# Kernel tuning notes

Measured on AMD Instinct MI355X. Metric: run time of the kernel, lower is better.

The kernel has to match this reference:

```python
import jax, jax.numpy as jnp
import numpy as np

EMBED_DIM = 1024
NUM_HEADS = 16
HEAD_DIM = EMBED_DIM // NUM_HEADS


def setup_inputs() -> dict:
    key = jax.random.key(0)
    ks = jax.random.split(key, 5)
    B, S, D = 2, 2048, EMBED_DIM
    scale_w = 1.0 / np.sqrt(D)
    x = jax.random.normal(ks[0], (B, S, D), dtype=jnp.float32)
    Wq = jax.random.normal(ks[1], (D, D), dtype=jnp.float32) * scale_w
    Wk = jax.random.normal(ks[2], (D, D), dtype=jnp.float32) * scale_w
    Wv = jax.random.normal(ks[3], (D, D), dtype=jnp.float32) * scale_w
    Wo = jax.random.normal(ks[4], (D, D), dtype=jnp.float32) * scale_w
    return {"x": x, "Wq": Wq, "Wk": Wk, "Wv": Wv, "Wo": Wo}


def reference(x, Wq, Wk, Wv, Wo):
    B, S, D = x.shape
    H, Dh = NUM_HEADS, HEAD_DIM
    scale = 1.0 / jnp.sqrt(jnp.asarray(Dh, dtype=x.dtype))

    def split_heads(t):
        return t.reshape(B, S, H, Dh).transpose(0, 2, 1, 3)  # [B,H,S,Dh]

    q = split_heads(x @ Wq)
    k = split_heads(x @ Wk)
    v = split_heads(x @ Wv)

    scores = jnp.einsum("bhqd,bhkd->bhqk", q, k) * scale
    causal = jnp.tril(jnp.ones((S, S), dtype=bool))[None, None]
    scores = jnp.where(causal, scores, jnp.asarray(-1e9, dtype=scores.dtype))
    weights = jax.nn.softmax(scores, axis=-1)
    attn = jnp.einsum("bhqk,bhkd->bhqd", weights, v)
    attn = attn.transpose(0, 2, 1, 3).reshape(B, S, D)
    return attn @ Wo
```

## Files before the change

kernel.cpp:

```cpp
#include <hip/hip_runtime.h>
#include <cstdint>

typedef __bf16 bf16;
typedef __bf16 bf16x2 __attribute__((ext_vector_type(2)));
typedef __bf16 bf16x4 __attribute__((ext_vector_type(4)));
typedef __bf16 bf16x8 __attribute__((ext_vector_type(8)));
typedef float f32x4 __attribute__((ext_vector_type(4)));

constexpr int S = 2048, D = 1024, H = 16, HD = 64, B = 2;
constexpr size_t TSZ = (size_t)B * H * S * HD;

__device__ __forceinline__ f32x4 mfma16(bf16x8 a, bf16x8 b, f32x4 c) {
  return __builtin_amdgcn_mfma_f32_16x16x32_bf16(a, b, c, 0, 0, 0);
}

__device__ __forceinline__ void gl_lds16(const bf16* g, bf16* s) {
  __builtin_amdgcn_global_load_lds((__attribute__((address_space(1))) void*)g,
                                   (__attribute__((address_space(3))) void*)s,
                                   16, 0, 0);
}

__global__ __launch_bounds__(256) void prep_all(const float* __restrict__ x,
                                                const float* __restrict__ W0,
                                                const float* __restrict__ W1,
                                                const float* __restrict__ W2,
                                                const float* __restrict__ W3,
                                                bf16* __restrict__ xb,
                                                bf16* __restrict__ Wt) {
  __shared__ __align__(16) bf16 Lt[64][68];
  const int bid = blockIdx.x, t = threadIdx.x;
  if (bid < 2048) {
    const size_t i = (size_t)bid * 256 + t;
    const float4 a = ((const float4*)x)[2 * i];
    const float4 b = ((const float4*)x)[2 * i + 1];
    bf16x8 o = {(bf16)a.x, (bf16)a.y, (bf16)a.z, (bf16)a.w,
                (bf16)b.x, (bf16)b.y, (bf16)b.z, (bf16)b.w};
    *(bf16x8*)&xb[i * 8] = o;
    return;
  }
  const int r = bid - 2048;
  const int z = r >> 8, rest = r & 255;
  const float* W = z == 0 ? W0 : z == 1 ? W1 : z == 2 ? W2 : W3;
  const int k0 = (rest & 15) * 64, n0 = (rest >> 4) * 64;
  const int tr = t >> 4, tc = (t & 15) * 4;
#pragma unroll
  for (int p = 0; p < 4; ++p) {
    const int rr = 16 * p + tr;
    const float4 v = *(const float4*)&W[(size_t)(k0 + rr) * D + n0 + tc];
    Lt[tc + 0][rr] = (bf16)v.x;
    Lt[tc + 1][rr] = (bf16)v.y;
    Lt[tc + 2][rr] = (bf16)v.z;
    Lt[tc + 3][rr] = (bf16)v.w;
  }
  __syncthreads();
#pragma unroll
  for (int p = 0; p < 4; ++p) {
    const int n = 16 * p + tr;
    const bf16x4 o = *(const bf16x4*)&Lt[n][tc];
    *(bf16x4*)&Wt[((size_t)z * D + n0 + n) * D + k0 + tc] = o;
  }
}

template <int MODE, int BNT>
__global__ __launch_bounds__(256) void gemm_bt(const bf16* __restrict__ A,
                                               const bf16* __restrict__ Bt,
                                               void* __restrict__ Cp) {
  constexpr int K = 1024;
  constexpr int NI = BNT / 32;
  __shared__ __align__(16) bf16 As[128 * 64];
  __shared__ __align__(16) bf16 Bs[BNT * 64];

  const int bid = blockIdx.x, nwg = gridDim.x;
  const int lg = (bid & 7) * (nwg >> 3) + (bid >> 3);
  const int bm = (lg & 31) * 128;
  const int bn = (lg >> 5) * BNT;

  const int t = threadIdx.x, l = t & 63, w = t >> 6;
  const int c = l & 15, g = l >> 4, cx = c & 7;
  const int lrow = l >> 3;
  const int srcc = ((l & 7) ^ lrow) << 3;
  const int wm = (w >> 1) * 64, wn = (w & 1) * (BNT / 2);

  f32x4 acc[4][NI] = {};

  for (int kt = 0; kt < K / 64; ++kt) {
    const int k0 = kt * 64;
    __syncthreads();
#pragma unroll
    for (int i = 0; i < 4; ++i) {
      const int ci = i * 4 + w;
      const int row = ci * 8 + lrow;
      gl_lds16(A + (size_t)(bm + row) * K + k0 + srcc, As + ci * 512 + l * 8);
    }
#pragma unroll
    for (int i = 0; i < BNT / 32; ++i) {
      const int ci = i * 4 + w;
      const int row = ci * 8 + lrow;
      gl_lds16(Bt + (size_t)(bn + row) * K + k0 + srcc, Bs + ci * 512 + l * 8);
    }
    __syncthreads();

    bf16x8 af[4][2], bfv[NI][2];
#pragma unroll
    for (int mi = 0; mi < 4; ++mi) {
      const int row = wm + mi * 16 + c;
#pragma unroll
      for (int kh = 0; kh < 2; ++kh)
        af[mi][kh] = *(const bf16x8*)&As[row * 64 + (((kh * 4 + g) ^ cx) << 3)];
    }
#pragma unroll
    for (int ni = 0; ni < NI; ++ni) {
      const int row = wn + ni * 16 + c;
#pragma unroll
      for (int kh = 0; kh < 2; ++kh)
        bfv[ni][kh] = *(const bf16x8*)&Bs[row * 64 + (((kh * 4 + g) ^ cx) << 3)];
    }
#pragma unroll
    for (int mi = 0; mi < 4; ++mi)
#pragma unroll
      for (int ni = 0; ni < NI; ++ni) {
        acc[mi][ni] = mfma16(af[mi][0], bfv[ni][0], acc[mi][ni]);
        acc[mi][ni] = mfma16(af[mi][1], bfv[ni][1], acc[mi][ni]);
      }
  }

#pragma unroll
  for (int mi = 0; mi < 4; ++mi)
#pragma unroll
    for (int ni = 0; ni < NI; ++ni)
#pragma unroll
      for (int r = 0; r < 4; ++r) {
        const int m = bm + wm + mi * 16 + 4 * g + r;
        const int n = bn + wn + ni * 16 + c;
        const float v = acc[mi][ni][r];
        if constexpr (MODE == 0) {
          const int which = n >> 10, nn = n & 1023;
          const int h = nn >> 6, d = nn & 63;
          const int bb = m >> 11, s = m & 2047;
          ((bf16*)Cp)[which * TSZ + ((((size_t)bb * H + h) * S + s) << 6) + d] =
              (bf16)v;
        } else {
          ((float*)Cp)[(size_t)m * D + n] = v;
        }
      }
}

__global__ __launch_bounds__(256, 4) void attn9(const bf16* __restrict__ Q,
                                                const bf16* __restrict__ Kg,
                                                const bf16* __restrict__ Vg,
                                                bf16* __restrict__ O) {
  __shared__ __align__(16) bf16 Ks[64 * 64];
  __shared__ __align__(16) bf16 Vt[64 * 64];
  __shared__ __align__(16) bf16 Pb[4][16 * 64];

  const int bid = blockIdx.x;
  const int qt = 31 - (bid >> 5);
  const int bh = bid & 31;
  const int t = threadIdx.x, l = t & 63, w = t >> 6;
  const int c = l & 15, g = l >> 4, cx = c & 7;
  const int bb = bh >> 4, h = bh & 15;
  const float SC = 0.18033688011112042f;
  const float THRS = 44.3614195558365f;

  const bf16* Kbase = Kg + (size_t)bh * S * HD;
  const bf16* Vbase = Vg + (size_t)bh * S * HD;

  const int q0 = qt * 64;
  const int qglob = q0 + 16 * w + c;
  const bf16* Qrow = Q + ((size_t)bh * S + qglob) * HD;
  const bf16x8 qf0 = *(const bf16x8*)&Qrow[g * 8];
  const bf16x8 qf1 = *(const bf16x8*)&Qrow[32 + g * 8];

  const int kv0 = t >> 3, dg0 = t & 7;
  const int kv1 = kv0 + 32;
  const int p2 = t & 31, dgv = t >> 5;

  bf16x8 ka0 = *(const bf16x8*)&Kbase[kv0 * 64 + dg0 * 8];
  bf16x8 ka1 = *(const bf16x8*)&Kbase[kv1 * 64 + dg0 * 8];
  bf16x8 va0 = *(const bf16x8*)&Vbase[(2 * p2) * 64 + dgv * 8];
  bf16x8 va1 = *(const bf16x8*)&Vbase[(2 * p2 + 1) * 64 + dgv * 8];

  f32x4 oacc[4] = {};
  float mrun = -1e30f, lrun = 0.f;

  for (int kt = 0; kt <= qt; ++kt) {
    __builtin_amdgcn_s_barrier();
    __builtin_amdgcn_sched_barrier(0);

    *(bf16x8*)&Ks[kv0 * 64 + ((dg0 ^ (kv0 & 7)) << 3)] = ka0;
    *(bf16x8*)&Ks[kv1 * 64 + ((dg0 ^ (kv1 & 7)) << 3)] = ka1;
#pragma unroll
    for (int i = 0; i < 8; ++i) {
      const int vd = 8 * dgv + i;
      bf16x2 pr2 = {va0[i], va1[i]};
      *(bf16x2*)&Vt[vd * 64 + (((p2 >> 2) ^ i) << 3) + ((p2 & 3) << 1)] = pr2;
    }
    bf16x8 kn0 = ka0, kn1 = ka1, vn0 = va0, vn1 = va1;
    if (kt < qt) {
      const bf16* Kt = Kbase + (size_t)(kt + 1) * 64 * HD;
      const bf16* Vs = Vbase + (size_t)(kt + 1) * 64 * HD;
      kn0 = *(const bf16x8*)&Kt[kv0 * 64 + dg0 * 8];
      kn1 = *(const bf16x8*)&Kt[kv1 * 64 + dg0 * 8];
      vn0 = *(const bf16x8*)&Vs[(2 * p2) * 64 + dgv * 8];
      vn1 = *(const bf16x8*)&Vs[(2 * p2 + 1) * 64 + dgv * 8];
    }
    asm volatile("s_waitcnt lgkmcnt(0)" ::: "memory");
    __builtin_amdgcn_s_barrier();
    __builtin_amdgcn_sched_barrier(0);

    f32x4 st[4];
    __builtin_amdgcn_s_setprio(1);
#pragma unroll
    for (int ct = 0; ct < 4; ++ct) {
      const int krow = ct * 16 + c;
      const bf16x8 kf0 = *(const bf16x8*)&Ks[krow * 64 + ((g ^ cx) << 3)];
      const bf16x8 kf1 = *(const bf16x8*)&Ks[krow * 64 + (((4 + g) ^ cx) << 3)];
      f32x4 z = {};
      z = mfma16(kf0, qf0, z);
      st[ct] = mfma16(kf1, qf1, z);
    }
    __builtin_amdgcn_s_setprio(0);

    if (kt == qt) {
#pragma unroll
      for (int ct = 0; ct < 4; ++ct)
#pragma unroll
        for (int r = 0; r < 4; ++r)
          if (kt * 64 + ct * 16 + 4 * g + r > qglob) st[ct][r] = -1e30f;
    }

    float tm[4];
#pragma unroll
    for (int ct = 0; ct < 4; ++ct)
      tm[ct] = fmaxf(fmaxf(st[ct][0], st[ct][1]), fmaxf(st[ct][2], st[ct][3]));
    float mt = fmaxf(fmaxf(tm[0], tm[1]), fmaxf(tm[2], tm[3]));
    mt = fmaxf(mt, __shfl_xor(mt, 16));
    mt = fmaxf(mt, __shfl_xor(mt, 32));
    if (!__all(mt <= mrun + THRS)) {
      const float mnew = fmaxf(mrun, mt);
      const float fac = __builtin_amdgcn_exp2f((mrun - mnew) * SC);
      lrun *= fac;
#pragma unroll
      for (int ct = 0; ct < 4; ++ct)
#pragma unroll
        for (int r = 0; r < 4; ++r) oacc[ct][r] *= fac;
      mrun = mnew;
    }
    float p[4][4];
    float sq[4];
#pragma unroll
    for (int ct = 0; ct < 4; ++ct) {
#pragma unroll
      for (int r = 0; r < 4; ++r)
        p[ct][r] = __builtin_amdgcn_exp2f((st[ct][r] - mrun) * SC);
      sq[ct] = (p[ct][0] + p[ct][1]) + (p[ct][2] + p[ct][3]);
    }
    lrun += (sq[0] + sq[1]) + (sq[2] + sq[3]);

    bf16* Pw = &Pb[w][0];
#pragma unroll
    for (int ct = 0; ct < 4; ++ct)
#pragma unroll
      for (int pr = 0; pr < 2; ++pr) {
        const int ch = (2 * ct + (g >> 1)) ^ cx;
        bf16x2 pk = {(bf16)p[ct][2 * pr], (bf16)p[ct][2 * pr + 1]};
        *(bf16x2*)&Pw[c * 64 + ch * 8 + (g & 1) * 4 + pr * 2] = pk;
      }
    const bf16x8 pa0 = *(const bf16x8*)&Pw[c * 64 + ((g ^ cx) << 3)];
    const bf16x8 pa1 = *(const bf16x8*)&Pw[c * 64 + (((4 + g) ^ cx) << 3)];

    __builtin_amdgcn_s_setprio(1);
#pragma unroll
    for (int ct = 0; ct < 4; ++ct) {
      const int vrow = ct * 16 + c;
      const bf16x8 vt0 = *(const bf16x8*)&Vt[vrow * 64 + ((g ^ cx) << 3)];
      const bf16x8 vt1 = *(const bf16x8*)&Vt[vrow * 64 + (((4 + g) ^ cx) << 3)];
      oacc[ct] = mfma16(vt0, pa0, oacc[ct]);
      oacc[ct] = mfma16(vt1, pa1, oacc[ct]);
    }
    __builtin_amdgcn_s_setprio(0);

    ka0 = kn0; ka1 = kn1; va0 = vn0; va1 = vn1;
  }

  float lt = lrun;
  lt += __shfl_xor(lt, 16);
  lt += __shfl_xor(lt, 32);
  const float inv = 1.f / lt;
  bf16* Orow = O + ((size_t)bb * S + qglob) * D + h * 64;
#pragma unroll
  for (int ct = 0; ct < 4; ++ct)
#pragma unroll
    for (int pr = 0; pr < 2; ++pr) {
      bf16x2 pk = {(bf16)(oacc[ct][2 * pr] * inv),
                   (bf16)(oacc[ct][2 * pr + 1] * inv)};
      *(bf16x2*)&Orow[ct * 16 + 4 * g + 2 * pr] = pk;
    }
}

extern "C" void kernel_launch(void* const* d_in, const int* in_sizes, int n_in,
                              void* d_out, int out_size, void* d_ws, size_t ws_size,
                              hipStream_t stream) {
  const float* x  = (const float*)d_in[0];
  const float* Wq = (const float*)d_in[1];
  const float* Wk = (const float*)d_in[2];
  const float* Wv = (const float*)d_in[3];
  const float* Wo = (const float*)d_in[4];
  float* out = (float*)d_out;

  bf16* xb  = (bf16*)d_ws;
  bf16* Wt  = xb + (size_t)B * S * D;
  bf16* QKV = Wt + (size_t)4 * D * D;
  bf16* Ab  = QKV + 3 * TSZ;

  prep_all<<<3072, 256, 0, stream>>>(x, Wq, Wk, Wv, Wo, xb, Wt);
  gemm_bt<0, 128><<<768, 256, 0, stream>>>(xb, Wt, QKV);
  attn9<<<1024, 256, 0, stream>>>(QKV, QKV + TSZ, QKV + 2 * TSZ, Ab);
  gemm_bt<1, 64><<<512, 256, 0, stream>>>(Ab, Wt + (size_t)3 * D * D, out);
}
```

Before: 100.5 us.

## Split long causal attention rows across two KV halves with a merge kernel

```diff
diff --git a/kernel.cpp b/kernel.cpp
--- a/kernel.cpp
+++ b/kernel.cpp
@@ -145,20 +145,22 @@
       }
 }
 
-__global__ __launch_bounds__(256, 4) void attn9(const bf16* __restrict__ Q,
-                                                const bf16* __restrict__ Kg,
-                                                const bf16* __restrict__ Vg,
-                                                bf16* __restrict__ O) {
+__global__ __launch_bounds__(256, 4) void attn10(const bf16* __restrict__ Q,
+                                                 const bf16* __restrict__ Kg,
+                                                 const bf16* __restrict__ Vg,
+                                                 float* __restrict__ Pp) {
   __shared__ __align__(16) bf16 Ks[64 * 64];
   __shared__ __align__(16) bf16 Vt[64 * 64];
-  __shared__ __align__(16) bf16 Pb[4][16 * 64];
 
   const int bid = blockIdx.x;
-  const int qt = 31 - (bid >> 5);
-  const int bh = bid & 31;
+  const int bh = bid & 31, e = bid >> 5;
+  int qt, kvA, kvB, half;
+  if (e < 16)      { qt = 31 - e; half = 0; kvA = 0;             kvB = (qt + 2) >> 1; }
+  else if (e < 32) { qt = 47 - e; half = 1; kvA = (qt + 2) >> 1; kvB = qt + 1; }
+  else             { qt = 47 - e; half = 0; kvA = 0;             kvB = qt + 1; }
+
   const int t = threadIdx.x, l = t & 63, w = t >> 6;
   const int c = l & 15, g = l >> 4, cx = c & 7;
-  const int bb = bh >> 4, h = bh & 15;
   const float SC = 0.18033688011112042f;
   const float THRS = 44.3614195558365f;
 
@@ -174,16 +176,22 @@
   const int kv0 = t >> 3, dg0 = t & 7;
   const int kv1 = kv0 + 32;
   const int p2 = t & 31, dgv = t >> 5;
-
-  bf16x8 ka0 = *(const bf16x8*)&Kbase[kv0 * 64 + dg0 * 8];
-  bf16x8 ka1 = *(const bf16x8*)&Kbase[kv1 * 64 + dg0 * 8];
-  bf16x8 va0 = *(const bf16x8*)&Vbase[(2 * p2) * 64 + dgv * 8];
-  bf16x8 va1 = *(const bf16x8*)&Vbase[(2 * p2 + 1) * 64 + dgv * 8];
+  const int hv = p2 >> 4;
+  const int gv = (p2 >> 1) & 3;
+  const int jv = ((p2 >> 3) & 1) * 4 + (p2 & 1) * 2;
+  const int vchunk = (hv << 2) | gv;
+
+  const bf16* K0 = Kbase + (size_t)kvA * 64 * HD;
+  const bf16* V0 = Vbase + (size_t)kvA * 64 * HD;
+  bf16x8 ka0 = *(const bf16x8*)&K0[kv0 * 64 + dg0 * 8];
+  bf16x8 ka1 = *(const bf16x8*)&K0[kv1 * 64 + dg0 * 8];
+  bf16x8 va0 = *(const bf16x8*)&V0[(2 * p2) * 64 + dgv * 8];
+  bf16x8 va1 = *(const bf16x8*)&V0[(2 * p2 + 1) * 64 + dgv * 8];
 
   f32x4 oacc[4] = {};
   float mrun = -1e30f, lrun = 0.f;
 
-  for (int kt = 0; kt <= qt; ++kt) {
+  for (int kt = kvA; kt < kvB; ++kt) {
     __builtin_amdgcn_s_barrier();
     __builtin_amdgcn_sched_barrier(0);
 
@@ -193,10 +201,10 @@
     for (int i = 0; i < 8; ++i) {
       const int vd = 8 * dgv + i;
       bf16x2 pr2 = {va0[i], va1[i]};
-      *(bf16x2*)&Vt[vd * 64 + (((p2 >> 2) ^ i) << 3) + ((p2 & 3) << 1)] = pr2;
+      *(bf16x2*)&Vt[vd * 64 + ((vchunk ^ i) << 3) + jv] = pr2;
     }
     bf16x8 kn0 = ka0, kn1 = ka1, vn0 = va0, vn1 = va1;
-    if (kt < qt) {
+    if (kt + 1 < kvB) {
       const bf16* Kt = Kbase + (size_t)(kt + 1) * 64 * HD;
       const bf16* Vs = Vbase + (size_t)(kt + 1) * 64 * HD;
       kn0 = *(const bf16x8*)&Kt[kv0 * 64 + dg0 * 8];
@@ -257,17 +265,10 @@
     }
     lrun += (sq[0] + sq[1]) + (sq[2] + sq[3]);
 
-    bf16* Pw = &Pb[w][0];
-#pragma unroll
-    for (int ct = 0; ct < 4; ++ct)
-#pragma unroll
-      for (int pr = 0; pr < 2; ++pr) {
-        const int ch = (2 * ct + (g >> 1)) ^ cx;
-        bf16x2 pk = {(bf16)p[ct][2 * pr], (bf16)p[ct][2 * pr + 1]};
-        *(bf16x2*)&Pw[c * 64 + ch * 8 + (g & 1) * 4 + pr * 2] = pk;
-      }
-    const bf16x8 pa0 = *(const bf16x8*)&Pw[c * 64 + ((g ^ cx) << 3)];
-    const bf16x8 pa1 = *(const bf16x8*)&Pw[c * 64 + (((4 + g) ^ cx) << 3)];
+    const bf16x8 pa0 = {(bf16)p[0][0], (bf16)p[0][1], (bf16)p[0][2], (bf16)p[0][3],
+                        (bf16)p[1][0], (bf16)p[1][1], (bf16)p[1][2], (bf16)p[1][3]};
+    const bf16x8 pa1 = {(bf16)p[2][0], (bf16)p[2][1], (bf16)p[2][2], (bf16)p[2][3],
+                        (bf16)p[3][0], (bf16)p[3][1], (bf16)p[3][2], (bf16)p[3][3]};
 
     __builtin_amdgcn_s_setprio(1);
 #pragma unroll
@@ -286,16 +287,33 @@
   float lt = lrun;
   lt += __shfl_xor(lt, 16);
   lt += __shfl_xor(lt, 32);
-  const float inv = 1.f / lt;
-  bf16* Orow = O + ((size_t)bb * S + qglob) * D + h * 64;
+  float* Pr = Pp + ((((size_t)bh * 32 + qt) * 2 + half) * 64 + 16 * w + c) * 68;
 #pragma unroll
   for (int ct = 0; ct < 4; ++ct)
-#pragma unroll
-    for (int pr = 0; pr < 2; ++pr) {
-      bf16x2 pk = {(bf16)(oacc[ct][2 * pr] * inv),
-                   (bf16)(oacc[ct][2 * pr + 1] * inv)};
-      *(bf16x2*)&Orow[ct * 16 + 4 * g + 2 * pr] = pk;
-    }
+    *(f32x4*)&Pr[16 * ct + 4 * g] = oacc[ct];
+  if (g == 0) { Pr[64] = mrun; Pr[65] = lt; }
+}
+
+__global__ __launch_bounds__(256) void attn_merge(const float* __restrict__ Pp,
+                                                  bf16* __restrict__ Ab) {
+  const float SC = 0.18033688011112042f;
+  const int gid = blockIdx.x * 4 + (threadIdx.x >> 6);
+  const int bh = gid >> 11, s = gid & 2047;
+  const int lane = threadIdx.x & 63;
+  const int qt = s >> 6, row = s & 63;
+  const float* r0 = Pp + ((((size_t)bh * 32 + qt) * 2 + 0) * 64 + row) * 68;
+  float o = r0[lane];
+  float m = r0[64], l = r0[65];
+  if (qt >= 16) {
+    const float* r1 = r0 + 64 * 68;
+    const float o1 = r1[lane], m1 = r1[64], l1 = r1[65];
+    const float mn = fmaxf(m, m1);
+    const float f0 = exp2f((m - mn) * SC), f1 = exp2f((m1 - mn) * SC);
+    o = o * f0 + o1 * f1;
+    l = l * f0 + l1 * f1;
+  }
+  const int bb = bh >> 4, h = bh & 15;
+  Ab[((size_t)bb * S + s) * D + h * 64 + lane] = (bf16)(o / l);
 }
 
 extern "C" void kernel_launch(void* const* d_in, const int* in_sizes, int n_in,
@@ -312,9 +330,11 @@
   bf16* Wt  = xb + (size_t)B * S * D;
   bf16* QKV = Wt + (size_t)4 * D * D;
   bf16* Ab  = QKV + 3 * TSZ;
+  float* Pp = (float*)(Ab + TSZ);
 
   prep_all<<<3072, 256, 0, stream>>>(x, Wq, Wk, Wv, Wo, xb, Wt);
   gemm_bt<0, 128><<<768, 256, 0, stream>>>(xb, Wt, QKV);
-  attn9<<<1024, 256, 0, stream>>>(QKV, QKV + TSZ, QKV + 2 * TSZ, Ab);
+  attn10<<<1536, 256, 0, stream>>>(QKV, QKV + TSZ, QKV + 2 * TSZ, Pp);
+  attn_merge<<<16384, 256, 0, stream>>>(Pp, Ab);
   gemm_bt<1, 64><<<512, 256, 0, stream>>>(Ab, Wt + (size_t)3 * D * D, out);
 }
```

Result: slower. 104.0 us (+3.5%).

## Pair causal query tiles per block and pass P via registers

Applied to the files above, without the earlier changes.

```diff
diff --git a/kernel.cpp b/kernel.cpp
--- a/kernel.cpp
+++ b/kernel.cpp
@@ -145,17 +145,15 @@
       }
 }
 
-__global__ __launch_bounds__(256, 4) void attn9(const bf16* __restrict__ Q,
-                                                const bf16* __restrict__ Kg,
-                                                const bf16* __restrict__ Vg,
-                                                bf16* __restrict__ O) {
+__global__ __launch_bounds__(256, 4) void attn11(const bf16* __restrict__ Q,
+                                                 const bf16* __restrict__ Kg,
+                                                 const bf16* __restrict__ Vg,
+                                                 bf16* __restrict__ O) {
   __shared__ __align__(16) bf16 Ks[64 * 64];
   __shared__ __align__(16) bf16 Vt[64 * 64];
-  __shared__ __align__(16) bf16 Pb[4][16 * 64];
 
   const int bid = blockIdx.x;
-  const int qt = 31 - (bid >> 5);
-  const int bh = bid & 31;
+  const int bh = bid & 31, j = bid >> 5;
   const int t = threadIdx.x, l = t & 63, w = t >> 6;
   const int c = l & 15, g = l >> 4, cx = c & 7;
   const int bb = bh >> 4, h = bh & 15;
@@ -165,137 +163,136 @@
   const bf16* Kbase = Kg + (size_t)bh * S * HD;
   const bf16* Vbase = Vg + (size_t)bh * S * HD;
 
-  const int q0 = qt * 64;
-  const int qglob = q0 + 16 * w + c;
-  const bf16* Qrow = Q + ((size_t)bh * S + qglob) * HD;
-  const bf16x8 qf0 = *(const bf16x8*)&Qrow[g * 8];
-  const bf16x8 qf1 = *(const bf16x8*)&Qrow[32 + g * 8];
-
   const int kv0 = t >> 3, dg0 = t & 7;
   const int kv1 = kv0 + 32;
   const int p2 = t & 31, dgv = t >> 5;
-
-  bf16x8 ka0 = *(const bf16x8*)&Kbase[kv0 * 64 + dg0 * 8];
-  bf16x8 ka1 = *(const bf16x8*)&Kbase[kv1 * 64 + dg0 * 8];
-  bf16x8 va0 = *(const bf16x8*)&Vbase[(2 * p2) * 64 + dgv * 8];
-  bf16x8 va1 = *(const bf16x8*)&Vbase[(2 * p2 + 1) * 64 + dgv * 8];
-
-  f32x4 oacc[4] = {};
-  float mrun = -1e30f, lrun = 0.f;
-
-  for (int kt = 0; kt <= qt; ++kt) {
-    __builtin_amdgcn_s_barrier();
-    __builtin_amdgcn_sched_barrier(0);
-
-    *(bf16x8*)&Ks[kv0 * 64 + ((dg0 ^ (kv0 & 7)) << 3)] = ka0;
-    *(bf16x8*)&Ks[kv1 * 64 + ((dg0 ^ (kv1 & 7)) << 3)] = ka1;
-#pragma unroll
-    for (int i = 0; i < 8; ++i) {
-      const int vd = 8 * dgv + i;
-      bf16x2 pr2 = {va0[i], va1[i]};
-      *(bf16x2*)&Vt[vd * 64 + (((p2 >> 2) ^ i) << 3) + ((p2 & 3) << 1)] = pr2;
-    }
-    bf16x8 kn0 = ka0, kn1 = ka1, vn0 = va0, vn1 = va1;
-    if (kt < qt) {
-      const bf16* Kt = Kbase + (size_t)(kt + 1) * 64 * HD;
-      const bf16* Vs = Vbase + (size_t)(kt + 1) * 64 * HD;
-      kn0 = *(const bf16x8*)&Kt[kv0 * 64 + dg0 * 8];
-      kn1 = *(const bf16x8*)&Kt[kv1 * 64 + dg0 * 8];
-      vn0 = *(const bf16x8*)&Vs[(2 * p2) * 64 + dgv * 8];
-      vn1 = *(const bf16x8*)&Vs[(2 * p2 + 1) * 64 + dgv * 8];
-    }
-    asm volatile("s_waitcnt lgkmcnt(0)" ::: "memory");
-    __builtin_amdgcn_s_barrier();
-    __builtin_amdgcn_sched_barrier(0);
-
-    f32x4 st[4];
-    __builtin_amdgcn_s_setprio(1);
-#pragma unroll
-    for (int ct = 0; ct < 4; ++ct) {
-      const int krow = ct * 16 + c;
-      const bf16x8 kf0 = *(const bf16x8*)&Ks[krow * 64 + ((g ^ cx) << 3)];
-      const bf16x8 kf1 = *(const bf16x8*)&Ks[krow * 64 + (((4 + g) ^ cx) << 3)];
-      f32x4 z = {};
-      z = mfma16(kf0, qf0, z);
-      st[ct] = mfma16(kf1, qf1, z);
-    }
-    __builtin_amdgcn_s_setprio(0);
-
-    if (kt == qt) {
+  const int hv = p2 >> 4;
+  const int gv = (p2 >> 1) & 3;
+  const int jv = ((p2 >> 3) & 1) * 4 + (p2 & 1) * 2;
+  const int vchunk = (hv << 2) | gv;
+
+  for (int ph = 0; ph < 2; ++ph) {
+    const int qt = ph ? (31 - j) : j;
+    const int q0 = qt * 64;
+    const int qglob = q0 + 16 * w + c;
+    const bf16* Qrow = Q + ((size_t)bh * S + qglob) * HD;
+    const bf16x8 qf0 = *(const bf16x8*)&Qrow[g * 8];
+    const bf16x8 qf1 = *(const bf16x8*)&Qrow[32 + g * 8];
+
+    bf16x8 ka0 = *(const bf16x8*)&Kbase[kv0 * 64 + dg0 * 8];
+    bf16x8 ka1 = *(const bf16x8*)&Kbase[kv1 * 64 + dg0 * 8];
+    bf16x8 va0 = *(const bf16x8*)&Vbase[(2 * p2) * 64 + dgv * 8];
+    bf16x8 va1 = *(const bf16x8*)&Vbase[(2 * p2 + 1) * 64 + dgv * 8];
+
+    f32x4 oacc[4] = {};
+    float mrun = -1e30f, lrun = 0.f;
+
+    for (int kt = 0; kt <= qt; ++kt) {
+      __builtin_amdgcn_s_barrier();
+      __builtin_amdgcn_sched_barrier(0);
+
+      *(bf16x8*)&Ks[kv0 * 64 + ((dg0 ^ (kv0 & 7)) << 3)] = ka0;
+      *(bf16x8*)&Ks[kv1 * 64 + ((dg0 ^ (kv1 & 7)) << 3)] = ka1;
+#pragma unroll
+      for (int i = 0; i < 8; ++i) {
+        bf16x2 pr2 = {va0[i], va1[i]};
+        *(bf16x2*)&Vt[(8 * dgv + i) * 64 + ((vchunk ^ i) << 3) + jv] = pr2;
+      }
+      bf16x8 kn0 = ka0, kn1 = ka1, vn0 = va0, vn1 = va1;
+      if (kt < qt) {
+        const bf16* Kt = Kbase + (size_t)(kt + 1) * 64 * HD;
+        const bf16* Vs = Vbase + (size_t)(kt + 1) * 64 * HD;
+        kn0 = *(const bf16x8*)&Kt[kv0 * 64 + dg0 * 8];
+        kn1 = *(const bf16x8*)&Kt[kv1 * 64 + dg0 * 8];
+        vn0 = *(const bf16x8*)&Vs[(2 * p2) * 64 + dgv * 8];
+        vn1 = *(const bf16x8*)&Vs[(2 * p2 + 1) * 64 + dgv * 8];
+      }
+      asm volatile("s_waitcnt lgkmcnt(0)" ::: "memory");
+      __builtin_amdgcn_s_barrier();
+      __builtin_amdgcn_sched_barrier(0);
+
+      f32x4 st[4];
+      __builtin_amdgcn_s_setprio(1);
+#pragma unroll
+      for (int ct = 0; ct < 4; ++ct) {
+        const int krow = ct * 16 + c;
+        const bf16x8 kf0 = *(const bf16x8*)&Ks[krow * 64 + ((g ^ cx) << 3)];
+        const bf16x8 kf1 = *(const bf16x8*)&Ks[krow * 64 + (((4 + g) ^ cx) << 3)];
+        f32x4 z = {};
+        z = mfma16(kf0, qf0, z);
+        st[ct] = mfma16(kf1, qf1, z);
+      }
+      __builtin_amdgcn_s_setprio(0);
+
+      if (kt == qt) {
+#pragma unroll
+        for (int ct = 0; ct < 4; ++ct)
+#pragma unroll
+          for (int r = 0; r < 4; ++r)
+            if (kt * 64 + ct * 16 + 4 * g + r > qglob) st[ct][r] = -1e30f;
+      }
+
+      float tm[4];
 #pragma unroll
       for (int ct = 0; ct < 4; ++ct)
+        tm[ct] = fmaxf(fmaxf(st[ct][0], st[ct][1]), fmaxf(st[ct][2], st[ct][3]));
+      float mt = fmaxf(fmaxf(tm[0], tm[1]), fmaxf(tm[2], tm[3]));
+      mt = fmaxf(mt, __shfl_xor(mt, 16));
+      mt = fmaxf(mt, __shfl_xor(mt, 32));
+      if (!__all(mt <= mrun + THRS)) {
+        const float mnew = fmaxf(mrun, mt);
+        const float fac = __builtin_amdgcn_exp2f((mrun - mnew) * SC);
+        lrun *= fac;
+#pragma unroll
+        for (int ct = 0; ct < 4; ++ct)
+#pragma unroll
+          for (int r = 0; r < 4; ++r) oacc[ct][r] *= fac;
+        mrun = mnew;
+      }
+      float p[4][4];
+      float sq[4];
+#pragma unroll
+      for (int ct = 0; ct < 4; ++ct) {
 #pragma unroll
         for (int r = 0; r < 4; ++r)
-          if (kt * 64 + ct * 16 + 4 * g + r > qglob) st[ct][r] = -1e30f;
-    }
-
-    float tm[4];
+          p[ct][r] = __builtin_amdgcn_exp2f((st[ct][r] - mrun) * SC);
+        sq[ct] = (p[ct][0] + p[ct][1]) + (p[ct][2] + p[ct][3]);
+      }
+      lrun += (sq[0] + sq[1]) + (sq[2] + sq[3]);
+
+      const bf16x8 pa0 = {(bf16)p[0][0], (bf16)p[0][1], (bf16)p[0][2], (bf16)p[0][3],
+                          (bf16)p[1][0], (bf16)p[1][1], (bf16)p[1][2], (bf16)p[1][3]};
+      const bf16x8 pa1 = {(bf16)p[2][0], (bf16)p[2][1], (bf16)p[2][2], (bf16)p[2][3],
+                          (bf16)p[3][0], (bf16)p[3][1], (bf16)p[3][2], (bf16)p[3][3]};
+
+      __builtin_amdgcn_s_setprio(1);
+#pragma unroll
+      for (int ct = 0; ct < 4; ++ct) {
+        const int vrow = ct * 16 + c;
+        const bf16x8 vt0 = *(const bf16x8*)&Vt[vrow * 64 + ((g ^ cx) << 3)];
+        const bf16x8 vt1 = *(const bf16x8*)&Vt[vrow * 64 + (((4 + g) ^ cx) << 3)];
+        oacc[ct] = mfma16(vt0, pa0, oacc[ct]);
+        oacc[ct] = mfma16(vt1, pa1, oacc[ct]);
+      }
+      __builtin_amdgcn_s_setprio(0);
+
+      ka0 = kn0; ka1 = kn1; va0 = vn0; va1 = vn1;
+    }
+
+    float lt = lrun;
+    lt += __shfl_xor(lt, 16);
+    lt += __shfl_xor(lt, 32);
+    const float inv = 1.f / lt;
+    bf16* Orow = O + ((size_t)bb * S + qglob) * D + h * 64;
 #pragma unroll
     for (int ct = 0; ct < 4; ++ct)
-      tm[ct] = fmaxf(fmaxf(st[ct][0], st[ct][1]), fmaxf(st[ct][2], st[ct][3]));
-    float mt = fmaxf(fmaxf(tm[0], tm[1]), fmaxf(tm[2], tm[3]));
-    mt = fmaxf(mt, __shfl_xor(mt, 16));
-    mt = fmaxf(mt, __shfl_xor(mt, 32));
-    if (!__all(mt <= mrun + THRS)) {
-      const float mnew = fmaxf(mrun, mt);
-      const float fac = __builtin_amdgcn_exp2f((mrun - mnew) * SC);
-      lrun *= fac;
-#pragma unroll
-      for (int ct = 0; ct < 4; ++ct)
-#pragma unroll
-        for (int r = 0; r < 4; ++r) oacc[ct][r] *= fac;
-      mrun = mnew;
-    }
-    float p[4][4];
-    float sq[4];
-#pragma unroll
-    for (int ct = 0; ct < 4; ++ct) {
-#pragma unroll
-      for (int r = 0; r < 4; ++r)
-        p[ct][r] = __builtin_amdgcn_exp2f((st[ct][r] - mrun) * SC);
-      sq[ct] = (p[ct][0] + p[ct][1]) + (p[ct][2] + p[ct][3]);
-    }
-    lrun += (sq[0] + sq[1]) + (sq[2] + sq[3]);
-
-    bf16* Pw = &Pb[w][0];
-#pragma unroll
-    for (int ct = 0; ct < 4; ++ct)
 #pragma unroll
       for (int pr = 0; pr < 2; ++pr) {
-        const int ch = (2 * ct + (g >> 1)) ^ cx;
-        bf16x2 pk = {(bf16)p[ct][2 * pr], (bf16)p[ct][2 * pr + 1]};
-        *(bf16x2*)&Pw[c * 64 + ch * 8 + (g & 1) * 4 + pr * 2] = pk;
-      }
-    const bf16x8 pa0 = *(const bf16x8*)&Pw[c * 64 + ((g ^ cx) << 3)];
-    const bf16x8 pa1 = *(const bf16x8*)&Pw[c * 64 + (((4 + g) ^ cx) << 3)];
-
-    __builtin_amdgcn_s_setprio(1);
-#pragma unroll
-    for (int ct = 0; ct < 4; ++ct) {
-      const int vrow = ct * 16 + c;
-      const bf16x8 vt0 = *(const bf16x8*)&Vt[vrow * 64 + ((g ^ cx) << 3)];
-      const bf16x8 vt1 = *(const bf16x8*)&Vt[vrow * 64 + (((4 + g) ^ cx) << 3)];
-      oacc[ct] = mfma16(vt0, pa0, oacc[ct]);
-      oacc[ct] = mfma16(vt1, pa1, oacc[ct]);
-    }
-    __builtin_amdgcn_s_setprio(0);
-
-    ka0 = kn0; ka1 = kn1; va0 = vn0; va1 = vn1;
-  }
-
-  float lt = lrun;
-  lt += __shfl_xor(lt, 16);
-  lt += __shfl_xor(lt, 32);
-  const float inv = 1.f / lt;
-  bf16* Orow = O + ((size_t)bb * S + qglob) * D + h * 64;
-#pragma unroll
-  for (int ct = 0; ct < 4; ++ct)
-#pragma unroll
-    for (int pr = 0; pr < 2; ++pr) {
-      bf16x2 pk = {(bf16)(oacc[ct][2 * pr] * inv),
-                   (bf16)(oacc[ct][2 * pr + 1] * inv)};
-      *(bf16x2*)&Orow[ct * 16 + 4 * g + 2 * pr] = pk;
-    }
+        bf16x2 pk = {(bf16)(oacc[ct][2 * pr] * inv),
+                     (bf16)(oacc[ct][2 * pr + 1] * inv)};
+        *(bf16x2*)&Orow[ct * 16 + 4 * g + 2 * pr] = pk;
+      }
+  }
 }
 
 extern "C" void kernel_launch(void* const* d_in, const int* in_sizes, int n_in,
@@ -315,6 +312,6 @@
 
   prep_all<<<3072, 256, 0, stream>>>(x, Wq, Wk, Wv, Wo, xb, Wt);
   gemm_bt<0, 128><<<768, 256, 0, stream>>>(xb, Wt, QKV);
-  attn9<<<1024, 256, 0, stream>>>(QKV, QKV + TSZ, QKV + 2 * TSZ, Ab);
+  attn11<<<512, 256, 0, stream>>>(QKV, QKV + TSZ, QKV + 2 * TSZ, Ab);
   gemm_bt<1, 64><<<512, 256, 0, stream>>>(Ab, Wt + (size_t)3 * D * D, out);
 }
```

Measured after the change: 98.56 us. Within noise of the previous version (-1.9%).
